# Kernel tuning notes

Hardware: AMD Instinct MI355X
Metric: run time of the kernel (lower is better)

Reference implementation:

```python
import jax, jax.numpy as jnp
import numpy as np
import math
from jax import lax

WINDOWS = (3, 5, 7)
GRIDSIZE = 3
HALF_H = 384  # hidden of each directional LSTM (d_model // 2)


def _lstm_last(x, mask, Wih, Whh, bih, bhh, reverse):
    """Masked single-layer LSTM; returns final hidden state.
    x: [N, T, D], mask: [N, T] bool. Invalid steps leave (h, c) unchanged,
    which is equivalent to running the LSTM only over the valid contiguous
    sub-window (leading/trailing pads are skipped).
    PyTorch gate order: i, f, g, o.
    """
    N = x.shape[0]
    H = Whh.shape[1]
    h0 = jnp.zeros((N, H), x.dtype)
    c0 = jnp.zeros((N, H), x.dtype)

    def step(carry, inp):
        h, c = carry
        xt, mt = inp
        gates = xt @ Wih.T + h @ Whh.T + (bih + bhh)
        i, f, g, o = jnp.split(gates, 4, axis=-1)
        i = jax.nn.sigmoid(i); f = jax.nn.sigmoid(f); o = jax.nn.sigmoid(o)
        g = jnp.tanh(g)
        c_new = f * c + i * g
        h_new = o * jnp.tanh(c_new)
        m = mt[:, None]
        return (jnp.where(m, h_new, h), jnp.where(m, c_new, c)), None

    xs = (jnp.moveaxis(x, 1, 0), jnp.moveaxis(mask, 1, 0))
    (h, _), _ = lax.scan(step, (h0, c0), xs, reverse=reverse)
    return h


def setup_inputs() -> dict:
    key = jax.random.key(0)
    ks = jax.random.split(key, 12)
    B, L, D = 16, 512, 768
    H4 = 4 * HALF_H
    s = 0.02
    inp = {
        'sequence_output': jax.random.normal(ks[0], (B, L, D), jnp.float32),
        'Wih_f': jax.random.normal(ks[1], (3, H4, D), jnp.float32) * s,
        'Whh_f': jax.random.normal(ks[2], (3, H4, HALF_H), jnp.float32) * s,
        'bih_f': jax.random.normal(ks[3], (3, H4), jnp.float32) * s,
        'bhh_f': jax.random.normal(ks[4], (3, H4), jnp.float32) * s,
        'Wih_b': jax.random.normal(ks[5], (3, H4, D), jnp.float32) * s,
        'Whh_b': jax.random.normal(ks[6], (3, H4, HALF_H), jnp.float32) * s,
        'bih_b': jax.random.normal(ks[7], (3, H4), jnp.float32) * s,
        'bhh_b': jax.random.normal(ks[8], (3, H4), jnp.float32) * s,
        'kan_coeffs': jax.random.normal(ks[9], (2, 11, GRIDSIZE, D), jnp.float32)
                      / (np.sqrt(D) * np.sqrt(GRIDSIZE)),
        'kan_bias': jax.random.normal(ks[10], (11,), jnp.float32) * s,
        'valid_ids': jax.random.randint(ks[11], (B, L), 0, 2, jnp.int64),
    }
    return inp


def reference(sequence_output, Wih_f, Whh_f, bih_f, bhh_f,
              Wih_b, Whh_b, bih_b, bhh_b, kan_coeffs, kan_bias, valid_ids):
    B, L, D = sequence_output.shape
    # ---- valid-id compaction (scatter valid tokens to the front, zeros after)
    v = valid_ids == 1
    dest = jnp.where(v, jnp.cumsum(v, axis=1) - 1, L)  # invalid -> dump slot L
    bidx = jnp.arange(B)[:, None]
    valid_output = (jnp.zeros((B, L + 1, D), sequence_output.dtype)
                    .at[bidx, dest].set(sequence_output))[:, :L]
    x = valid_output  # dropout is identity in eval

    # ---- per-window sliding BiLSTM (vectorized over all B*L positions)
    outs = []
    for wi, w in enumerate(WINDOWS):
        half = w // 2
        idx = jnp.arange(L)[:, None] + jnp.arange(-half, half + 1)[None, :]  # [L,w]
        valid = (idx >= 0) & (idx < L)
        idxc = jnp.clip(idx, 0, L - 1)
        xw = x[:, idxc].reshape(B * L, w, D)                  # [B*L, w, D]
        m = jnp.broadcast_to(valid[None], (B, L, w)).reshape(B * L, w)
        hf = _lstm_last(xw, m, Wih_f[wi], Whh_f[wi], bih_f[wi], bhh_f[wi], False)
        hb = _lstm_last(xw, m, Wih_b[wi], Whh_b[wi], bih_b[wi], bhh_b[wi], True)
        outs.append(jnp.concatenate([hf, hb], axis=-1).reshape(B, L, D))

    seq = outs[0] + outs[1] + outs[2]

    # ---- 'dot-att' fusion over window features
    stk = jnp.stack(outs, axis=2)                             # [B, L, K, D]
    q = seq[:, :, None, :]                                    # [B, L, 1, D]
    attn = jax.nn.softmax(
        jnp.einsum('blqd,blkd->blqk', q, stk) / math.sqrt(D), axis=-1)
    local = jnp.einsum('blqk,blkd->blqd', attn, stk)[:, :, 0]
    seq = seq + local

    # ---- NaiveFourierKAN classifier (gridsize=3)
    k = jnp.arange(1, GRIDSIZE + 1, dtype=seq.dtype)
    xg = seq[..., None, :] * k[:, None]                       # [B, L, g, D]
    logits = (jnp.einsum('blgi,ogi->blo', jnp.cos(xg), kan_coeffs[0])
              + jnp.einsum('blgi,ogi->blo', jnp.sin(xg), kan_coeffs[1])
              + kan_bias)
    return logits
```

## Files before the change

kernel.cpp:

```cpp
#include <hip/hip_runtime.h>

#define BT 8192
#define SEQL 512
#define DIM 768
#define HID 384
#define NG 1536

using US = unsigned short;
typedef __bf16 bf16x8 __attribute__((ext_vector_type(8)));
typedef float f32x4 __attribute__((ext_vector_type(4)));

__device__ __forceinline__ float b2f(US u) {
  union { unsigned u; float f; } x; x.u = ((unsigned)u) << 16; return x.f;
}
__device__ __forceinline__ US f2b(float f) {
  __bf16 h = (__bf16)f;
  union { __bf16 h; US u; } x; x.h = h; return x.u;
}
__device__ __forceinline__ float fsig(float x) { return 1.f / (1.f + __expf(-x)); }
__device__ __forceinline__ float ftanh(float x) { return 1.f - 2.f / (__expf(2.f * x) + 1.f); }

__device__ __forceinline__ size_t pk_off(int panel, int rloc, int col, int panelStride) {
  return (size_t)panel * panelStride + (col >> 6) * 8192 + ((col >> 5) & 1) * 4096 +
         (rloc >> 6) * 2048 + ((rloc >> 4) & 3) * 512 +
         (((rloc & 15) | (((col & 31) >> 3) << 4))) * 8 + (col & 7);
}

__global__ __launch_bounds__(256) void convW_ih_k(const float* __restrict__ WihF,
                                                  const float* __restrict__ WihB,
                                                  US* __restrict__ WihP) {
  int d = blockIdx.z;
  const float* src = d ? WihB : WihF;
  size_t idx = (size_t)blockIdx.x * 256 + threadIdx.x;
  int lane = (int)(idx & 63);
  int t = (int)(idx >> 6);
  int sg = t & 3;
  int wn = (t >> 2) & 1;
  int kk = (t >> 3) & 1;
  int kt = (t >> 4) % 12;
  int nb = (t / 192) % 12;
  int wi = t / (192 * 12);
  int srow = sg * HID + nb * 32 + wn * 16 + (lane & 15);
  int scol = kt * 64 + kk * 32 + (lane >> 4) * 8;
  const float* s = src + ((size_t)wi * NG + srow) * DIM + scol;
  float4 v0 = *(const float4*)s;
  float4 v1 = *(const float4*)(s + 4);
  ushort4 o0, o1;
  o0.x = f2b(v0.x); o0.y = f2b(v0.y); o0.z = f2b(v0.z); o0.w = f2b(v0.w);
  o1.x = f2b(v1.x); o1.y = f2b(v1.y); o1.z = f2b(v1.z); o1.w = f2b(v1.w);
  US* dst = WihP + ((size_t)d * 442368 + idx) * 8;
  *(ushort4*)dst = o0;
  *(ushort4*)(dst + 4) = o1;
}

__global__ __launch_bounds__(256) void convW_hh_k(const float* __restrict__ WhhF,
                                                  const float* __restrict__ WhhB,
                                                  US* __restrict__ WhhP) {
  int d = blockIdx.z;
  const float* src = d ? WhhB : WhhF;
  size_t idx = (size_t)blockIdx.x * 256 + threadIdx.x;
  int lane = (int)(idx & 63);
  int t = (int)(idx >> 6);
  int sg = t & 3;
  int wn = (t >> 2) & 1;
  int kk = (t >> 3) & 1;
  int kt = (t >> 4) % 6;
  int hb = (t / 96) % 12;
  int wi = t / (96 * 12);
  int srow = sg * HID + hb * 32 + wn * 16 + (lane & 15);
  int scol = kt * 64 + kk * 32 + (lane >> 4) * 8;
  const float* s = src + ((size_t)wi * NG + srow) * HID + scol;
  float4 v0 = *(const float4*)s;
  float4 v1 = *(const float4*)(s + 4);
  ushort4 o0, o1;
  o0.x = f2b(v0.x); o0.y = f2b(v0.y); o0.z = f2b(v0.z); o0.w = f2b(v0.w);
  o1.x = f2b(v1.x); o1.y = f2b(v1.y); o1.z = f2b(v1.z); o1.w = f2b(v1.w);
  US* dst = WhhP + ((size_t)d * 221184 + idx) * 8;
  *(ushort4*)dst = o0;
  *(ushort4*)(dst + 4) = o1;
}

__global__ __launch_bounds__(256) void conv_coef_k(const float* __restrict__ coef,
                                                   US* __restrict__ coefP) {
  int idx = blockIdx.x * 256 + threadIdx.x;
  int s = idx & 31;
  int i = (idx >> 5) % DIM;
  int g = idx / (32 * DIM);
  float v = 0.f;
  int o = s & 15;
  if (o < 11) v = coef[(size_t)((s >> 4) * 33 + o * 3 + g) * DIM + i];
  coefP[idx] = f2b(v);
}

__global__ void scan_k(const int* __restrict__ valid, int* __restrict__ dest) {
  __shared__ int s[SEQL];
  int b = blockIdx.x, l = threadIdx.x;
  int v = (valid[b * SEQL + l] == 1) ? 1 : 0;
  s[l] = v;
  __syncthreads();
  for (int off = 1; off < SEQL; off <<= 1) {
    int t = (l >= off) ? s[l - off] : 0;
    __syncthreads();
    s[l] += t;
    __syncthreads();
  }
  dest[b * SEQL + l] = v ? (s[l] - 1) : -1;
}

__global__ __launch_bounds__(256) void scatter_k(const float* __restrict__ seq,
                                                 const int* __restrict__ dest,
                                                 US* __restrict__ xcP) {
  int idx = blockIdx.x * 256 + threadIdx.x;
  int p = idx / 192, cc = idx - p * 192;
  int d = dest[p];
  if (d < 0) return;
  int b = p >> 9;
  float4 v = ((const float4*)seq)[(size_t)p * 192 + cc];
  ushort4 o;
  o.x = f2b(v.x); o.y = f2b(v.y); o.z = f2b(v.z); o.w = f2b(v.w);
  int pdst = b * SEQL + d;
  int c = cc * 4;
  size_t off = pk_off(pdst >> 7, pdst & 127, c, 98304);
  *(ushort4*)&xcP[off] = o;
}

__global__ __launch_bounds__(256, 4) void gate_gemm_k(
    const US* __restrict__ xcP, const US* __restrict__ WihP,
    const float* __restrict__ bihF, const float* __restrict__ bihB,
    const float* __restrict__ bhhF, const float* __restrict__ bhhB,
    US* __restrict__ G, int dirBase) {
  int zi = blockIdx.z;
  int wi = zi % 3, dr = dirBase + zi / 3;
  const float* bih = dr ? bihB : bihF;
  const float* bhh = dr ? bhhB : bhhF;
  int panel = blockIdx.x, nb = blockIdx.y;
  const US* Wp = WihP + ((size_t)(dr * 3 + wi) * 12 + nb) * 98304;
  US* Gw = G + (size_t)wi * BT * NG;
  __shared__ float biasS[128];
  int tid = threadIdx.x, lane = tid & 63, wid = tid >> 6;
  int wm = wid >> 1, wn = wid & 1;
  if (tid < 128) {
    int sg = tid >> 5, hl = tid & 31;
    int gc = wi * NG + sg * HID + nb * 32 + hl;
    biasS[tid] = bih[gc] + bhh[gc];
  }
  __syncthreads();
  f32x4 acc[4][4] = {};
  const US* Ab = xcP + (size_t)panel * 98304 + (size_t)wm * 2048 + (size_t)lane * 8;
  const US* Bb = Wp + (size_t)wn * 2048 + (size_t)lane * 8;
#pragma unroll 2
  for (int kp = 0; kp < 24; ++kp) {
    bf16x8 a[4], b[4];
    const US* ap = Ab + (size_t)kp * 4096;
    const US* bp = Bb + (size_t)kp * 4096;
#pragma unroll
    for (int mi = 0; mi < 4; ++mi) a[mi] = *(const bf16x8*)(ap + (size_t)mi * 512);
#pragma unroll
    for (int sg = 0; sg < 4; ++sg) b[sg] = *(const bf16x8*)(bp + (size_t)sg * 512);
#pragma unroll
    for (int mi = 0; mi < 4; ++mi)
#pragma unroll
      for (int sg = 0; sg < 4; ++sg)
        acc[mi][sg] = __builtin_amdgcn_mfma_f32_16x16x32_bf16(a[mi], b[sg], acc[mi][sg], 0, 0, 0);
  }
  int hh = wn * 16 + (lane & 15);
  int hidx = nb * 32 + hh;
  int m0 = panel * 128;
#pragma unroll
  for (int mi = 0; mi < 4; ++mi) {
#pragma unroll
    for (int r = 0; r < 4; ++r) {
      int p = m0 + wm * 64 + mi * 16 + ((lane >> 4) << 2) + r;
      ushort4 gv;
      gv.x = f2b(acc[mi][0][r] + biasS[hh]);
      gv.y = f2b(acc[mi][1][r] + biasS[32 + hh]);
      gv.z = f2b(acc[mi][2][r] + biasS[64 + hh]);
      gv.w = f2b(acc[mi][3][r] + biasS[96 + hh]);
      *(ushort4*)&Gw[(size_t)p * NG + (size_t)hidx * 4] = gv;
    }
  }
}

__global__ __launch_bounds__(384) void step0_k(const US* __restrict__ G, US* __restrict__ C,
                                               US* __restrict__ hn, int dirBase) {
  int zi = blockIdx.z;
  int wi = zi % 3, dr = dirBase + zi / 3;
  int half = wi + 1;
  int dlt = dr ? half : -half;
  int p = blockIdx.x, hidx = threadIdx.x;
  int l = p & (SEQL - 1);
  const US* Gw = G + (size_t)wi * BT * NG;
  float c = 0.f, h = 0.f;
  int t = l + dlt;
  if ((unsigned)t < (unsigned)SEQL) {
    ushort4 gv = *(const ushort4*)&Gw[(size_t)(p + dlt) * NG + (size_t)hidx * 4];
    c = fsig(b2f(gv.x)) * ftanh(b2f(gv.z));
    h = fsig(b2f(gv.w)) * ftanh(c);
  }
  C[(size_t)wi * BT * HID + (size_t)p * HID + hidx] = f2b(c);
  hn[(size_t)wi * BT * HID + pk_off(p >> 7, p & 127, hidx, 49152)] = f2b(h);
}

__global__ __launch_bounds__(256, 4) void step_k(
    const US* __restrict__ WhhP,
    const US* __restrict__ G, US* __restrict__ C,
    const US* __restrict__ hcur, US* __restrict__ hnxt, US* __restrict__ Outs,
    int s, int wi0, int nact, int dirBase) {
  int zi = blockIdx.z;
  int wi = wi0 + zi % nact, dr = dirBase + zi / nact;
  int w = 2 * wi + 3, half = wi + 1;
  int j = dr ? (w - 1 - s) : s;
  int dlt = j - half;
  bool fin = (s == w - 1);
  const US* Gw = G + (size_t)wi * BT * NG;
  US* Cw = C + (size_t)wi * BT * HID;
  const US* hc = hcur + (size_t)wi * BT * HID;
  US* hn = hnxt + (size_t)wi * BT * HID;
  US* Ow = Outs + (size_t)wi * BT * DIM + (dr ? HID : 0);
  int panel = blockIdx.x, hb = blockIdx.y;
  const US* Wp = WhhP + ((size_t)(dr * 3 + wi) * 12 + hb) * 49152;
  int tid = threadIdx.x, lane = tid & 63, wid = tid >> 6;
  int wm = wid >> 1, wn = wid & 1;
  f32x4 acc[4][4] = {};

  const US* Ab = hc + (size_t)panel * 49152 + (size_t)wm * 2048 + (size_t)lane * 8;
  const US* Bb = Wp + (size_t)wn * 2048 + (size_t)lane * 8;
#pragma unroll 2
  for (int kp = 0; kp < 12; ++kp) {
    bf16x8 a[4], b[4];
    const US* ap = Ab + (size_t)kp * 4096;
    const US* bp = Bb + (size_t)kp * 4096;
#pragma unroll
    for (int mi = 0; mi < 4; ++mi) a[mi] = *(const bf16x8*)(ap + (size_t)mi * 512);
#pragma unroll
    for (int sg = 0; sg < 4; ++sg) b[sg] = *(const bf16x8*)(bp + (size_t)sg * 512);
#pragma unroll
    for (int mi = 0; mi < 4; ++mi)
#pragma unroll
      for (int sg = 0; sg < 4; ++sg)
        acc[mi][sg] = __builtin_amdgcn_mfma_f32_16x16x32_bf16(a[mi], b[sg], acc[mi][sg], 0, 0, 0);
  }
  int l15 = lane & 15, l4 = lane >> 4;
  int hh = wn * 16 + l15;
  int hidx = hb * 32 + hh;
  int m0 = panel * 128;
  size_t wbase = (size_t)panel * 49152 + (size_t)hb * 4096 + (size_t)wm * 2048 +
                 (size_t)(wn * 2 + (l15 >> 3)) * 128 + (l15 & 7);
#pragma unroll
  for (int mi = 0; mi < 4; ++mi) {
#pragma unroll
    for (int r = 0; r < 4; ++r) {
      int p = m0 + wm * 64 + mi * 16 + (l4 << 2) + r;
      int l = p & (SEQL - 1);
      size_t po = wbase + (size_t)mi * 512 + (size_t)((l4 << 2) + r) * 8;
      float hval;
      if ((unsigned)(l + dlt) < (unsigned)SEQL) {
        ushort4 gv = *(const ushort4*)&Gw[(size_t)(p + dlt) * NG + (size_t)hidx * 4];
        float gi = acc[mi][0][r] + b2f(gv.x);
        float gf = acc[mi][1][r] + b2f(gv.y);
        float gg = acc[mi][2][r] + b2f(gv.z);
        float go = acc[mi][3][r] + b2f(gv.w);
        size_t ci = (size_t)p * HID + hidx;
        float c = fsig(gf) * b2f(Cw[ci]) + fsig(gi) * ftanh(gg);
        Cw[ci] = f2b(c);
        hval = fsig(go) * ftanh(c);
      } else {
        hval = b2f(hc[po]);
      }
      if (fin) Ow[(size_t)p * DIM + hidx] = f2b(hval);
      else hn[po] = f2b(hval);
    }
  }
}

__global__ __launch_bounds__(256) void attn_kan_k(
    const US* __restrict__ Outs, const US* __restrict__ coefP,
    const float* __restrict__ kbias, float* __restrict__ out) {
  int p4 = blockIdx.x * 4;
  int tid = threadIdx.x, lane = tid & 63, wid = tid >> 6;
  __shared__ float red[176];
  float sq[3][4];
  {
    float o0[3][4], o1[3][4], o2[3][4], q[3][4];
#pragma unroll
    for (int c = 0; c < 3; ++c) {
      int i = tid + 256 * c;
#pragma unroll
      for (int t = 0; t < 4; ++t) {
        o0[c][t] = b2f(Outs[(size_t)(p4 + t) * DIM + i]);
        o1[c][t] = b2f(Outs[(size_t)(BT + p4 + t) * DIM + i]);
        o2[c][t] = b2f(Outs[(size_t)(2 * BT + p4 + t) * DIM + i]);
        q[c][t] = o0[c][t] + o1[c][t] + o2[c][t];
      }
    }
    float d[3][4];
#pragma unroll
    for (int t = 0; t < 4; ++t) {
      d[0][t] = 0.f; d[1][t] = 0.f; d[2][t] = 0.f;
#pragma unroll
      for (int c = 0; c < 3; ++c) {
        d[0][t] += q[c][t] * o0[c][t];
        d[1][t] += q[c][t] * o1[c][t];
        d[2][t] += q[c][t] * o2[c][t];
      }
    }
#pragma unroll
    for (int off = 32; off; off >>= 1)
#pragma unroll
      for (int t = 0; t < 4; ++t) {
        d[0][t] += __shfl_down(d[0][t], off);
        d[1][t] += __shfl_down(d[1][t], off);
        d[2][t] += __shfl_down(d[2][t], off);
      }
    if (lane == 0)
#pragma unroll
      for (int t = 0; t < 4; ++t) {
        red[(t * 3 + 0) * 4 + wid] = d[0][t];
        red[(t * 3 + 1) * 4 + wid] = d[1][t];
        red[(t * 3 + 2) * 4 + wid] = d[2][t];
      }
    __syncthreads();
    const float scl = 0.03608439182435161f;
#pragma unroll
    for (int t = 0; t < 4; ++t) {
      float s0 = (red[(t * 3) * 4] + red[(t * 3) * 4 + 1] + red[(t * 3) * 4 + 2] + red[(t * 3) * 4 + 3]) * scl;
      float s1 = (red[(t * 3 + 1) * 4] + red[(t * 3 + 1) * 4 + 1] + red[(t * 3 + 1) * 4 + 2] + red[(t * 3 + 1) * 4 + 3]) * scl;
      float s2 = (red[(t * 3 + 2) * 4] + red[(t * 3 + 2) * 4 + 1] + red[(t * 3 + 2) * 4 + 2] + red[(t * 3 + 2) * 4 + 3]) * scl;
      float mx = fmaxf(s0, fmaxf(s1, s2));
      float a0 = __expf(s0 - mx), a1 = __expf(s1 - mx), a2 = __expf(s2 - mx);
      float inv = 1.f / (a0 + a1 + a2);
      a0 *= inv; a1 *= inv; a2 *= inv;
#pragma unroll
      for (int c = 0; c < 3; ++c)
        sq[c][t] = q[c][t] + a0 * o0[c][t] + a1 * o1[c][t] + a2 * o2[c][t];
    }
  }
  float acc[11][4];
#pragma unroll
  for (int o = 0; o < 11; ++o)
#pragma unroll
    for (int t = 0; t < 4; ++t) acc[o][t] = 0.f;
#pragma unroll
  for (int c = 0; c < 3; ++c) {
    int i = tid + 256 * c;
#pragma unroll
    for (int g = 0; g < 3; ++g) {
      float sn[4], cs[4];
#pragma unroll
      for (int t = 0; t < 4; ++t) __sincosf(sq[c][t] * (float)(g + 1), &sn[t], &cs[t]);
      const US* cp = coefP + ((size_t)g * DIM + i) * 32;
      bf16x8 k0 = *(const bf16x8*)(cp);
      bf16x8 k1 = *(const bf16x8*)(cp + 8);
      bf16x8 k2 = *(const bf16x8*)(cp + 16);
      bf16x8 k3 = *(const bf16x8*)(cp + 24);
#pragma unroll
      for (int o = 0; o < 8; ++o) {
        float cc = (float)k0[o], ss = (float)k2[o];
#pragma unroll
        for (int t = 0; t < 4; ++t) acc[o][t] += cs[t] * cc + sn[t] * ss;
      }
#pragma unroll
      for (int o = 8; o < 11; ++o) {
        float cc = (float)k1[o - 8], ss = (float)k3[o - 8];
#pragma unroll
        for (int t = 0; t < 4; ++t) acc[o][t] += cs[t] * cc + sn[t] * ss;
      }
    }
  }
  __syncthreads();
#pragma unroll
  for (int o = 0; o < 11; ++o)
#pragma unroll
    for (int t = 0; t < 4; ++t) {
      float v = acc[o][t];
#pragma unroll
      for (int off = 32; off; off >>= 1) v += __shfl_down(v, off);
      if (lane == 0) red[(o * 4 + t) * 4 + wid] = v;
    }
  __syncthreads();
  if (tid < 44) {
    int o = tid >> 2, t = tid & 3;
    out[(size_t)(p4 + t) * 11 + o] =
        red[tid * 4] + red[tid * 4 + 1] + red[tid * 4 + 2] + red[tid * 4 + 3] + kbias[o];
  }
}

extern "C" void kernel_launch(void* const* d_in, const int* in_sizes, int n_in,
                              void* d_out, int out_size, void* d_ws, size_t ws_size,
                              hipStream_t stream) {
  const float* seq = (const float*)d_in[0];
  const float* WihF = (const float*)d_in[1];
  const float* WhhF = (const float*)d_in[2];
  const float* bihF = (const float*)d_in[3];
  const float* bhhF = (const float*)d_in[4];
  const float* WihB = (const float*)d_in[5];
  const float* WhhB = (const float*)d_in[6];
  const float* bihB = (const float*)d_in[7];
  const float* bhhB = (const float*)d_in[8];
  const float* coef = (const float*)d_in[9];
  const float* kbias = (const float*)d_in[10];
  const int* valid = (const int*)d_in[11];

  constexpr size_t SZ_XC = (size_t)BT * DIM * 2;
  constexpr size_t SZ_DEST = (size_t)BT * 4;
  constexpr size_t SZ_CP = (size_t)3 * DIM * 32 * 2;
  constexpr size_t SZ_G = (size_t)3 * BT * NG * 2;
  constexpr size_t SZ_C = (size_t)3 * BT * HID * 2;
  constexpr size_t SZ_H = (size_t)3 * BT * HID * 2;
  constexpr size_t SZ_OUTS = (size_t)3 * BT * DIM * 2;
  constexpr size_t SZ_WIHP = (size_t)2 * 3 * NG * DIM * 2;
  constexpr size_t SZ_WHHP = (size_t)2 * 3 * NG * HID * 2;
  constexpr size_t NEED = SZ_XC + SZ_DEST + SZ_CP + SZ_WIHP + SZ_WHHP +
                          SZ_G + SZ_C + 2 * SZ_H + SZ_OUTS;
  if (ws_size < NEED) return;

  char* ws = (char*)d_ws;
  US* xcP = (US*)ws;                         ws += SZ_XC;
  int* dest = (int*)ws;                      ws += SZ_DEST;
  US* coefP = (US*)ws;                       ws += SZ_CP;
  US* WihP = (US*)ws;                        ws += SZ_WIHP;
  US* WhhP = (US*)ws;                        ws += SZ_WHHP;
  US* G = (US*)ws;                           ws += SZ_G;
  US* C = (US*)ws;                           ws += SZ_C;
  US* h0 = (US*)ws;                          ws += SZ_H;
  US* h1 = (US*)ws;                          ws += SZ_H;
  US* Outs = (US*)ws;
  float* out = (float*)d_out;

  hipMemsetAsync(xcP, 0, SZ_XC, stream);
  scan_k<<<16, SEQL, 0, stream>>>(valid, dest);
  scatter_k<<<(BT * 192) / 256, 256, 0, stream>>>(seq, dest, xcP);
  conv_coef_k<<<288, 256, 0, stream>>>(coef, coefP);
  convW_ih_k<<<dim3(442368 / 256, 1, 2), 256, 0, stream>>>(WihF, WihB, WihP);
  convW_hh_k<<<dim3(221184 / 256, 1, 2), 256, 0, stream>>>(WhhF, WhhB, WhhP);

  for (int dir = 0; dir < 2; ++dir) {
    gate_gemm_k<<<dim3(64, 12, 3), 256, 0, stream>>>(xcP, WihP, bihF, bihB, bhhF, bhhB, G, dir);
    step0_k<<<dim3(BT, 1, 3), HID, 0, stream>>>(G, C, h1, dir);
    for (int s = 1; s < 7; ++s) {
      int nact = (s < 3) ? 3 : ((s < 5) ? 2 : 1);
      int wi0 = 3 - nact;
      US* hcur = (s & 1) ? h1 : h0;
      US* hnxt = (s & 1) ? h0 : h1;
      step_k<<<dim3(64, 12, nact), 256, 0, stream>>>(WhhP, G, C, hcur, hnxt, Outs,
                                                     s, wi0, nact, dir);
    }
  }
  attn_kan_k<<<BT / 4, 256, 0, stream>>>(Outs, coefP, kbias, out);
}
```

Measured before the change: 805.6 us.

## Batch both LSTM directions into single launches and rework KAN reduction

When the workspace is large enough, the forward and backward directions get separate G/C/h buffers and run together in one gate GEMM, one step0 and one set of step launches, doubling grid z. This halves the number of small sequential launches and raises per-launch occupancy. Outs is aliased over the xc/Wih region, which is safe only because those inputs are dead by the final step. The attn_kan epilogue now writes per-thread partials to a padded LDS array and reduces them with float4 reads, replacing 44 wave-shuffle reductions at the cost of a much larger LDS footprint.

```diff
diff --git a/kernel.cpp b/kernel.cpp
--- a/kernel.cpp
+++ b/kernel.cpp
@@ -128,14 +128,14 @@
     const US* __restrict__ xcP, const US* __restrict__ WihP,
     const float* __restrict__ bihF, const float* __restrict__ bihB,
     const float* __restrict__ bhhF, const float* __restrict__ bhhB,
-    US* __restrict__ G, int dirBase) {
+    US* __restrict__ G, int dirBase, size_t gStr) {
   int zi = blockIdx.z;
-  int wi = zi % 3, dr = dirBase + zi / 3;
+  int wi = zi % 3, drz = zi / 3, dr = dirBase + drz;
   const float* bih = dr ? bihB : bihF;
   const float* bhh = dr ? bhhB : bhhF;
   int panel = blockIdx.x, nb = blockIdx.y;
   const US* Wp = WihP + ((size_t)(dr * 3 + wi) * 12 + nb) * 98304;
-  US* Gw = G + (size_t)wi * BT * NG;
+  US* Gw = G + (size_t)drz * gStr + (size_t)wi * BT * NG;
   __shared__ float biasS[128];
   int tid = threadIdx.x, lane = tid & 63, wid = tid >> 6;
   int wm = wid >> 1, wn = wid & 1;
@@ -182,14 +182,15 @@
 }
 
 __global__ __launch_bounds__(384) void step0_k(const US* __restrict__ G, US* __restrict__ C,
-                                               US* __restrict__ hn, int dirBase) {
+                                               US* __restrict__ hn, int dirBase,
+                                               size_t gStr, size_t cStr, size_t hStr) {
   int zi = blockIdx.z;
-  int wi = zi % 3, dr = dirBase + zi / 3;
+  int wi = zi % 3, drz = zi / 3, dr = dirBase + drz;
   int half = wi + 1;
   int dlt = dr ? half : -half;
   int p = blockIdx.x, hidx = threadIdx.x;
   int l = p & (SEQL - 1);
-  const US* Gw = G + (size_t)wi * BT * NG;
+  const US* Gw = G + (size_t)drz * gStr + (size_t)wi * BT * NG;
   float c = 0.f, h = 0.f;
   int t = l + dlt;
   if ((unsigned)t < (unsigned)SEQL) {
@@ -197,25 +198,26 @@
     c = fsig(b2f(gv.x)) * ftanh(b2f(gv.z));
     h = fsig(b2f(gv.w)) * ftanh(c);
   }
-  C[(size_t)wi * BT * HID + (size_t)p * HID + hidx] = f2b(c);
-  hn[(size_t)wi * BT * HID + pk_off(p >> 7, p & 127, hidx, 49152)] = f2b(h);
+  C[(size_t)drz * cStr + (size_t)wi * BT * HID + (size_t)p * HID + hidx] = f2b(c);
+  hn[(size_t)drz * hStr + (size_t)wi * BT * HID + pk_off(p >> 7, p & 127, hidx, 49152)] = f2b(h);
 }
 
 __global__ __launch_bounds__(256, 4) void step_k(
     const US* __restrict__ WhhP,
     const US* __restrict__ G, US* __restrict__ C,
     const US* __restrict__ hcur, US* __restrict__ hnxt, US* __restrict__ Outs,
-    int s, int wi0, int nact, int dirBase) {
+    int s, int wi0, int nact, int dirBase,
+    size_t gStr, size_t cStr, size_t hStr) {
   int zi = blockIdx.z;
-  int wi = wi0 + zi % nact, dr = dirBase + zi / nact;
+  int wi = wi0 + zi % nact, drz = zi / nact, dr = dirBase + drz;
   int w = 2 * wi + 3, half = wi + 1;
   int j = dr ? (w - 1 - s) : s;
   int dlt = j - half;
   bool fin = (s == w - 1);
-  const US* Gw = G + (size_t)wi * BT * NG;
-  US* Cw = C + (size_t)wi * BT * HID;
-  const US* hc = hcur + (size_t)wi * BT * HID;
-  US* hn = hnxt + (size_t)wi * BT * HID;
+  const US* Gw = G + (size_t)drz * gStr + (size_t)wi * BT * NG;
+  US* Cw = C + (size_t)drz * cStr + (size_t)wi * BT * HID;
+  const US* hc = hcur + (size_t)drz * hStr + (size_t)wi * BT * HID;
+  US* hn = hnxt + (size_t)drz * hStr + (size_t)wi * BT * HID;
   US* Ow = Outs + (size_t)wi * BT * DIM + (dr ? HID : 0);
   int panel = blockIdx.x, hb = blockIdx.y;
   const US* Wp = WhhP + ((size_t)(dr * 3 + wi) * 12 + hb) * 49152;
@@ -273,12 +275,13 @@
   }
 }
 
+#define RSTR 260
 __global__ __launch_bounds__(256) void attn_kan_k(
     const US* __restrict__ Outs, const US* __restrict__ coefP,
     const float* __restrict__ kbias, float* __restrict__ out) {
   int p4 = blockIdx.x * 4;
   int tid = threadIdx.x, lane = tid & 63, wid = tid >> 6;
-  __shared__ float red[176];
+  __shared__ float lds[44 * RSTR];
   float sq[3][4];
   {
     float o0[3][4], o1[3][4], o2[3][4], q[3][4];
@@ -315,17 +318,17 @@
     if (lane == 0)
 #pragma unroll
       for (int t = 0; t < 4; ++t) {
-        red[(t * 3 + 0) * 4 + wid] = d[0][t];
-        red[(t * 3 + 1) * 4 + wid] = d[1][t];
-        red[(t * 3 + 2) * 4 + wid] = d[2][t];
+        lds[(t * 3 + 0) * 4 + wid] = d[0][t];
+        lds[(t * 3 + 1) * 4 + wid] = d[1][t];
+        lds[(t * 3 + 2) * 4 + wid] = d[2][t];
       }
     __syncthreads();
     const float scl = 0.03608439182435161f;
 #pragma unroll
     for (int t = 0; t < 4; ++t) {
-      float s0 = (red[(t * 3) * 4] + red[(t * 3) * 4 + 1] + red[(t * 3) * 4 + 2] + red[(t * 3) * 4 + 3]) * scl;
-      float s1 = (red[(t * 3 + 1) * 4] + red[(t * 3 + 1) * 4 + 1] + red[(t * 3 + 1) * 4 + 2] + red[(t * 3 + 1) * 4 + 3]) * scl;
-      float s2 = (red[(t * 3 + 2) * 4] + red[(t * 3 + 2) * 4 + 1] + red[(t * 3 + 2) * 4 + 2] + red[(t * 3 + 2) * 4 + 3]) * scl;
+      float s0 = (lds[(t * 3) * 4] + lds[(t * 3) * 4 + 1] + lds[(t * 3) * 4 + 2] + lds[(t * 3) * 4 + 3]) * scl;
+      float s1 = (lds[(t * 3 + 1) * 4] + lds[(t * 3 + 1) * 4 + 1] + lds[(t * 3 + 1) * 4 + 2] + lds[(t * 3 + 1) * 4 + 3]) * scl;
+      float s2 = (lds[(t * 3 + 2) * 4] + lds[(t * 3 + 2) * 4 + 1] + lds[(t * 3 + 2) * 4 + 2] + lds[(t * 3 + 2) * 4 + 3]) * scl;
       float mx = fmaxf(s0, fmaxf(s1, s2));
       float a0 = __expf(s0 - mx), a1 = __expf(s1 - mx), a2 = __expf(s2 - mx);
       float inv = 1.f / (a0 + a1 + a2);
@@ -371,17 +374,25 @@
 #pragma unroll
   for (int o = 0; o < 11; ++o)
 #pragma unroll
-    for (int t = 0; t < 4; ++t) {
-      float v = acc[o][t];
-#pragma unroll
-      for (int off = 32; off; off >>= 1) v += __shfl_down(v, off);
-      if (lane == 0) red[(o * 4 + t) * 4 + wid] = v;
-    }
+    for (int t = 0; t < 4; ++t)
+      lds[(o * 4 + t) * RSTR + tid] = acc[o][t];
   __syncthreads();
-  if (tid < 44) {
-    int o = tid >> 2, t = tid & 3;
-    out[(size_t)(p4 + t) * 11 + o] =
-        red[tid * 4] + red[tid * 4 + 1] + red[tid * 4 + 2] + red[tid * 4 + 3] + kbias[o];
+  if (tid < 176) {
+    int r = tid >> 2, qq = tid & 3;
+    const float4* pv = (const float4*)&lds[r * RSTR + qq * 64];
+    float4 s4 = pv[0];
+#pragma unroll
+    for (int k = 1; k < 16; ++k) {
+      float4 v = pv[k];
+      s4.x += v.x; s4.y += v.y; s4.z += v.z; s4.w += v.w;
+    }
+    float v = (s4.x + s4.y) + (s4.z + s4.w);
+    v += __shfl_down(v, 1);
+    v += __shfl_down(v, 2);
+    if (qq == 0) {
+      int o = r >> 2, t = r & 3;
+      out[(size_t)(p4 + t) * 11 + o] = v + kbias[o];
+    }
   }
 }
 
@@ -404,27 +415,52 @@
   constexpr size_t SZ_XC = (size_t)BT * DIM * 2;
   constexpr size_t SZ_DEST = (size_t)BT * 4;
   constexpr size_t SZ_CP = (size_t)3 * DIM * 32 * 2;
-  constexpr size_t SZ_G = (size_t)3 * BT * NG * 2;
-  constexpr size_t SZ_C = (size_t)3 * BT * HID * 2;
-  constexpr size_t SZ_H = (size_t)3 * BT * HID * 2;
+  constexpr size_t SZ_G1 = (size_t)3 * BT * NG * 2;
+  constexpr size_t SZ_C1 = (size_t)3 * BT * HID * 2;
+  constexpr size_t SZ_H1 = (size_t)3 * BT * HID * 2;
   constexpr size_t SZ_OUTS = (size_t)3 * BT * DIM * 2;
   constexpr size_t SZ_WIHP = (size_t)2 * 3 * NG * DIM * 2;
   constexpr size_t SZ_WHHP = (size_t)2 * 3 * NG * HID * 2;
-  constexpr size_t NEED = SZ_XC + SZ_DEST + SZ_CP + SZ_WIHP + SZ_WHHP +
-                          SZ_G + SZ_C + 2 * SZ_H + SZ_OUTS;
-  if (ws_size < NEED) return;
+  constexpr size_t GE = (size_t)3 * BT * NG;
+  constexpr size_t CE = (size_t)3 * BT * HID;
+  constexpr size_t HE = (size_t)3 * BT * HID;
+
+  constexpr size_t NEED1 = SZ_XC + SZ_DEST + SZ_CP + SZ_WIHP + SZ_WHHP +
+                           SZ_G1 + SZ_C1 + 2 * SZ_H1 + SZ_OUTS;
+  constexpr size_t UNION = (SZ_XC + SZ_WIHP > SZ_OUTS) ? (SZ_XC + SZ_WIHP) : SZ_OUTS;
+  constexpr size_t NEED2 = UNION + SZ_DEST + SZ_CP + SZ_WHHP +
+                           2 * SZ_G1 + 2 * SZ_C1 + 4 * SZ_H1;
+  if (ws_size < NEED1) return;
+  const int ndir = (ws_size >= NEED2) ? 2 : 1;
 
   char* ws = (char*)d_ws;
-  US* xcP = (US*)ws;                         ws += SZ_XC;
-  int* dest = (int*)ws;                      ws += SZ_DEST;
-  US* coefP = (US*)ws;                       ws += SZ_CP;
-  US* WihP = (US*)ws;                        ws += SZ_WIHP;
-  US* WhhP = (US*)ws;                        ws += SZ_WHHP;
-  US* G = (US*)ws;                           ws += SZ_G;
-  US* C = (US*)ws;                           ws += SZ_C;
-  US* h0 = (US*)ws;                          ws += SZ_H;
-  US* h1 = (US*)ws;                          ws += SZ_H;
-  US* Outs = (US*)ws;
+  US *xcP, *coefP, *WihP, *WhhP, *G, *C, *h0, *h1, *Outs;
+  int* dest;
+  if (ndir == 2) {
+    xcP = (US*)ws;
+    WihP = (US*)(ws + SZ_XC);
+    Outs = (US*)ws;
+    char* p = ws + UNION;
+    dest = (int*)p;                    p += SZ_DEST;
+    coefP = (US*)p;                    p += SZ_CP;
+    WhhP = (US*)p;                     p += SZ_WHHP;
+    G = (US*)p;                        p += 2 * SZ_G1;
+    C = (US*)p;                        p += 2 * SZ_C1;
+    h0 = (US*)p;                       p += 2 * SZ_H1;
+    h1 = (US*)p;
+  } else {
+    char* p = ws;
+    xcP = (US*)p;                      p += SZ_XC;
+    dest = (int*)p;                    p += SZ_DEST;
+    coefP = (US*)p;                    p += SZ_CP;
+    WihP = (US*)p;                     p += SZ_WIHP;
+    WhhP = (US*)p;                     p += SZ_WHHP;
+    G = (US*)p;                        p += SZ_G1;
+    C = (US*)p;                        p += SZ_C1;
+    h0 = (US*)p;                       p += SZ_H1;
+    h1 = (US*)p;                       p += SZ_H1;
+    Outs = (US*)p;
+  }
   float* out = (float*)d_out;
 
   hipMemsetAsync(xcP, 0, SZ_XC, stream);
@@ -434,16 +470,31 @@
   convW_ih_k<<<dim3(442368 / 256, 1, 2), 256, 0, stream>>>(WihF, WihB, WihP);
   convW_hh_k<<<dim3(221184 / 256, 1, 2), 256, 0, stream>>>(WhhF, WhhB, WhhP);
 
-  for (int dir = 0; dir < 2; ++dir) {
-    gate_gemm_k<<<dim3(64, 12, 3), 256, 0, stream>>>(xcP, WihP, bihF, bihB, bhhF, bhhB, G, dir);
-    step0_k<<<dim3(BT, 1, 3), HID, 0, stream>>>(G, C, h1, dir);
+  if (ndir == 2) {
+    gate_gemm_k<<<dim3(64, 12, 6), 256, 0, stream>>>(xcP, WihP, bihF, bihB, bhhF, bhhB,
+                                                     G, 0, GE);
+    step0_k<<<dim3(BT, 1, 6), HID, 0, stream>>>(G, C, h1, 0, GE, CE, HE);
     for (int s = 1; s < 7; ++s) {
       int nact = (s < 3) ? 3 : ((s < 5) ? 2 : 1);
       int wi0 = 3 - nact;
       US* hcur = (s & 1) ? h1 : h0;
       US* hnxt = (s & 1) ? h0 : h1;
-      step_k<<<dim3(64, 12, nact), 256, 0, stream>>>(WhhP, G, C, hcur, hnxt, Outs,
-                                                     s, wi0, nact, dir);
+      step_k<<<dim3(64, 12, nact * 2), 256, 0, stream>>>(WhhP, G, C, hcur, hnxt, Outs,
+                                                         s, wi0, nact, 0, GE, CE, HE);
+    }
+  } else {
+    for (int dir = 0; dir < 2; ++dir) {
+      gate_gemm_k<<<dim3(64, 12, 3), 256, 0, stream>>>(xcP, WihP, bihF, bihB, bhhF, bhhB,
+                                                       G, dir, 0);
+      step0_k<<<dim3(BT, 1, 3), HID, 0, stream>>>(G, C, h1, dir, 0, 0, 0);
+      for (int s = 1; s < 7; ++s) {
+        int nact = (s < 3) ? 3 : ((s < 5) ? 2 : 1);
+        int wi0 = 3 - nact;
+        US* hcur = (s & 1) ? h1 : h0;
+        US* hnxt = (s & 1) ? h0 : h1;
+        step_k<<<dim3(64, 12, nact), 256, 0, stream>>>(WhhP, G, C, hcur, hnxt, Outs,
+                                                       s, wi0, nact, dir, 0, 0, 0);
+      }
     }
   }
   attn_kan_k<<<BT / 4, 256, 0, stream>>>(Outs, coefP, kbias, out);
```

Result: faster. 764.9 us (-5.1%).
